# Kernel optimization log

Hardware: AMD Instinct MI355X
Metric: run time of the kernel (lower is better)

## Reference

```python
import jax, jax.numpy as jnp
import numpy as np

N_NODES = 50000


def gcn_conv(x, W, b, src, dst, n):
    # dense transform first (as PyG GCNConv does), then sparse aggregate
    h = x @ W  # [N, out]
    # add self loops
    loop = jnp.arange(n, dtype=src.dtype)
    s = jnp.concatenate([src, loop])
    d = jnp.concatenate([dst, loop])
    # symmetric normalization: deg over targets with unit edge weights
    deg = jax.ops.segment_sum(jnp.ones_like(d, dtype=h.dtype), d, num_segments=n)
    dinv = jnp.where(deg > 0, jax.lax.rsqrt(deg), 0.0)
    norm = dinv[s] * dinv[d]  # [E+N]
    msg = h[s] * norm[:, None]  # gather + scale
    out = jax.ops.segment_sum(msg, d, num_segments=n)  # scatter-add
    return out + b


def setup_inputs() -> dict:
    key = jax.random.key(0)
    k1, k2, k3, k4, k5 = jax.random.split(key, 5)
    in_dim, hid, out_dim = 256, 128, 16
    x = jax.random.normal(k1, (N_NODES, in_dim), dtype=jnp.float32)
    edge_index = jax.random.randint(k2, (2, 800000), 0, N_NODES, dtype=jnp.int64)
    # Glorot-style init for GCNConv weights, zero bias (PyG default)
    W1 = jax.random.normal(k3, (in_dim, hid), dtype=jnp.float32) / np.sqrt(in_dim)
    b1 = jnp.zeros((hid,), dtype=jnp.float32)
    W2 = jax.random.normal(k4, (hid, out_dim), dtype=jnp.float32) / np.sqrt(hid)
    b2 = jnp.zeros((out_dim,), dtype=jnp.float32)
    return {"x": x, "edge_index": edge_index, "W1": W1, "b1": b1, "W2": W2, "b2": b2}


def reference(x, edge_index, W1, b1, W2, b2):
    # eval-mode forward: dropout is identity
    src, dst = edge_index[0], edge_index[1]
    n = x.shape[0]
    h = gcn_conv(x, W1, b1, src, dst, n)
    h = jax.nn.relu(h)
    h = gcn_conv(h, W2, b2, src, dst, n)
    return jax.nn.log_softmax(h, axis=1)
```

## Files before the change

### kernel.cpp

```cpp
#include <hip/hip_runtime.h>
#include <hip/hip_bf16.h>

#define N_NODES 50000
#define E_EDGES 800000
#define IN_DIM  256
#define HID     128
#define OUT_DIM 16

#define NBUCK 391
#define NBLK  128
#define P2CAP 4096

using frag_ab = __attribute__((ext_vector_type(8))) short;
using frag_cd = __attribute__((ext_vector_type(4))) float;

static __device__ inline short f2bf(float f) {
    union { float f; unsigned u; } v; v.f = f;
    unsigned r = (v.u + 0x7fffu + ((v.u >> 16) & 1u)) >> 16;
    return (short)r;
}
static __device__ inline float bflo(unsigned u) {
    union { unsigned u; float f; } v; v.u = u << 16; return v.f;
}
static __device__ inline float bfhi(unsigned u) {
    union { unsigned u; float f; } v; v.u = u & 0xffff0000u; return v.f;
}
static __device__ inline unsigned packbf(float a, float b) {
    return (unsigned)(unsigned short)f2bf(a) | ((unsigned)(unsigned short)f2bf(b) << 16);
}


__global__ __launch_bounds__(256) void csr_a(const int4* __restrict__ dst4,
                                             int* __restrict__ cnt_bb) {
    __shared__ int h[NBUCK];
    int t = threadIdx.x;
    for (int i = t; i < NBUCK; i += 256) h[i] = 0;
    __syncthreads();
    for (int i = blockIdx.x * 256 + t; i < E_EDGES / 4; i += NBLK * 256) {
        int4 d = dst4[i];
        atomicAdd(&h[d.x >> 7], 1);
        atomicAdd(&h[d.y >> 7], 1);
        atomicAdd(&h[d.z >> 7], 1);
        atomicAdd(&h[d.w >> 7], 1);
    }
    __syncthreads();
    for (int i = t; i < NBUCK; i += 256) cnt_bb[i * NBLK + blockIdx.x] = h[i];
}

__global__ __launch_bounds__(NBLK) void csr_b1(int* __restrict__ cnt_bb,
                                               int* __restrict__ btot) {
    __shared__ int sm[NBLK];
    int b = blockIdx.x, t = threadIdx.x;
    int v = cnt_bb[b * NBLK + t];
    sm[t] = v;
    __syncthreads();
    for (int o = 1; o < NBLK; o <<= 1) {
        int u = (t >= o) ? sm[t - o] : 0;
        __syncthreads();
        sm[t] += u;
        __syncthreads();
    }
    cnt_bb[b * NBLK + t] = sm[t] - v;
    if (t == NBLK - 1) btot[b] = sm[t];
}

__global__ __launch_bounds__(512) void csr_b2(const int* __restrict__ btot,
                                              int* __restrict__ bbase) {
    __shared__ int sm[512];
    int t = threadIdx.x;
    int v = (t < NBUCK) ? btot[t] : 0;
    sm[t] = v;
    __syncthreads();
    for (int o = 1; o < 512; o <<= 1) {
        int u = (t >= o) ? sm[t - o] : 0;
        __syncthreads();
        sm[t] += u;
        __syncthreads();
    }
    if (t < NBUCK) bbase[t] = sm[t] - v;
    if (t == 511) bbase[NBUCK] = sm[511];
}

__global__ __launch_bounds__(256) void csr_c(const int4* __restrict__ src4,
                                             const int4* __restrict__ dst4,
                                             const int* __restrict__ cnt_bb,
                                             const int* __restrict__ bbase,
                                             unsigned* __restrict__ tmp) {
    __shared__ int run[NBUCK];
    int t = threadIdx.x;
    for (int i = t; i < NBUCK; i += 256)
        run[i] = bbase[i] + cnt_bb[i * NBLK + blockIdx.x];
    __syncthreads();
    for (int i = blockIdx.x * 256 + t; i < E_EDGES / 4; i += NBLK * 256) {
        int4 d = dst4[i];
        int4 s = src4[i];
        int p0 = atomicAdd(&run[d.x >> 7], 1);
        tmp[p0] = (unsigned)s.x | ((unsigned)(d.x & 127) << 17);
        int p1 = atomicAdd(&run[d.y >> 7], 1);
        tmp[p1] = (unsigned)s.y | ((unsigned)(d.y & 127) << 17);
        int p2 = atomicAdd(&run[d.z >> 7], 1);
        tmp[p2] = (unsigned)s.z | ((unsigned)(d.z & 127) << 17);
        int p3 = atomicAdd(&run[d.w >> 7], 1);
        tmp[p3] = (unsigned)s.w | ((unsigned)(d.w & 127) << 17);
    }
}

__global__ __launch_bounds__(256) void csr_p2(const unsigned* __restrict__ tmp,
                                              const int* __restrict__ bbase,
                                              int* __restrict__ rowptr,
                                              float* __restrict__ dinv,
                                              int* __restrict__ ssrc) {
    __shared__ unsigned ed[P2CAP];
    __shared__ int cnt[128];
    __shared__ int off[128];
    int b = blockIdx.x, t = threadIdx.x;
    int base = bbase[b];
    int m = bbase[b + 1] - base;
    if (m > P2CAP) m = P2CAP;
    if (t < 128) cnt[t] = 0;
    __syncthreads();
    for (int i = t; i < m; i += 256) {
        unsigned v = tmp[base + i];
        ed[i] = v;
        atomicAdd(&cnt[v >> 17], 1);
    }
    __syncthreads();
    if (t < 128) off[t] = cnt[t];
    __syncthreads();
    for (int o = 1; o < 128; o <<= 1) {
        int u = (t >= o && t < 128) ? off[t - o] : 0;
        __syncthreads();
        if (t < 128) off[t] += u;
        __syncthreads();
    }
    if (t < 128) {
        int node = b * 128 + t;
        int ex = off[t] - cnt[t];
        if (node < N_NODES) {
            rowptr[node] = base + ex;
            dinv[node] = rsqrtf((float)(cnt[t] + 1));
        }
        off[t] = ex;
    }
    if (b == NBUCK - 1 && t == 0) rowptr[N_NODES] = E_EDGES;
    __syncthreads();
    for (int i = t; i < m; i += 256) {
        unsigned v = ed[i];
        int p = atomicAdd(&off[v >> 17], 1);
        ssrc[base + p] = (int)(v & 0x1FFFF);
    }
}

__global__ void w1_transpose(const float* __restrict__ W, uint4* __restrict__ wtf) {
    int j = blockIdx.x * blockDim.x + threadIdx.x;
    if (j >= 64 * 64) return;
    int f = j >> 6, lane = j & 63;
    int kt = f >> 3, t = f & 7;
    int m = lane & 15, q = lane >> 4;
    int c = t * 16 + m;
    int k0 = kt * 32 + q * 8;
    unsigned p[4];
#pragma unroll
    for (int i = 0; i < 4; ++i)
        p[i] = packbf(W[(k0 + 2 * i) * HID + c], W[(k0 + 2 * i + 1) * HID + c]);
    uint4 v; v.x = p[0]; v.y = p[1]; v.z = p[2]; v.w = p[3];
    wtf[j] = v;
}

__global__ __launch_bounds__(512) void gemm1_mfma(const float* __restrict__ x,
                                                  const uint4* __restrict__ wtf,
                                                  const float* __restrict__ dinv,
                                                  short* __restrict__ h) {
    __shared__ uint4 lwt[64 * 64];
    int tid = threadIdx.x;
#pragma unroll
    for (int i = 0; i < 8; ++i)
        lwt[i * 512 + tid] = wtf[i * 512 + tid];

    int wave = tid >> 6;
    int lane = tid & 63;
    int m = lane & 15;
    int q = lane >> 4;
    int row0 = blockIdx.x * 128 + wave * 16;
    int arow_idx = row0 + m;
    const float4* arow4 = (const float4*)(x + (size_t)(arow_idx < N_NODES ? arow_idx : 0) * IN_DIM);

    frag_ab a[8];
#pragma unroll
    for (int kt = 0; kt < 8; ++kt) {
        float4 f0 = arow4[kt * 8 + q * 2];
        float4 f1 = arow4[kt * 8 + q * 2 + 1];
        a[kt][0] = f2bf(f0.x); a[kt][1] = f2bf(f0.y); a[kt][2] = f2bf(f0.z); a[kt][3] = f2bf(f0.w);
        a[kt][4] = f2bf(f1.x); a[kt][5] = f2bf(f1.y); a[kt][6] = f2bf(f1.z); a[kt][7] = f2bf(f1.w);
    }

    frag_cd acc[8];
#pragma unroll
    for (int t = 0; t < 8; ++t) acc[t] = frag_cd{0.f, 0.f, 0.f, 0.f};

    __syncthreads();

#pragma unroll
    for (int kt = 0; kt < 8; ++kt) {
#pragma unroll
        for (int t = 0; t < 8; ++t) {
            frag_ab b = *(const frag_ab*)&lwt[(kt * 8 + t) * 64 + lane];
            acc[t] = __builtin_amdgcn_mfma_f32_16x16x32_bf16(a[kt], b, acc[t], 0, 0, 0);
        }
    }

    float dv[4];
#pragma unroll
    for (int r = 0; r < 4; ++r) {
        int orow = row0 + q * 4 + r;
        dv[r] = (orow < N_NODES) ? dinv[orow] : 0.f;
    }
#pragma unroll
    for (int t = 0; t < 8; ++t) {
#pragma unroll
        for (int r = 0; r < 4; ++r) {
            int orow = row0 + q * 4 + r;
            if (orow < N_NODES)
                h[(size_t)orow * HID + t * 16 + m] = f2bf(acc[t][r] * dv[r]);
        }
    }
}

__global__ __launch_bounds__(256) void agg1_pull(const short* __restrict__ h1s,
                                                 const float* __restrict__ dinv,
                                                 const float* __restrict__ b1,
                                                 const int* __restrict__ rowptr,
                                                 const int* __restrict__ ssrc,
                                                 unsigned* __restrict__ out1) {
    int wave = threadIdx.x >> 6;
    int lane = threadIdx.x & 63;
    int node = __builtin_amdgcn_readfirstlane(blockIdx.x * 4 + wave);
    if (node >= N_NODES) return;
    int eo = lane >> 4;
    int g  = lane & 15;

    int lo = rowptr[node], hi = rowptr[node + 1];
    float a0 = 0.f, a1 = 0.f, a2 = 0.f, a3 = 0.f;
    float a4 = 0.f, a5 = 0.f, a6 = 0.f, a7 = 0.f;

    if (eo == 0) {
        uint4 u = *(const uint4*)(h1s + (size_t)node * HID + g * 8);
        a0 = bflo(u.x); a1 = bfhi(u.x); a2 = bflo(u.y); a3 = bfhi(u.y);
        a4 = bflo(u.z); a5 = bfhi(u.z); a6 = bflo(u.w); a7 = bfhi(u.w);
    }

    int e = lo;
#pragma unroll 2
    for (; e + 4 <= hi; e += 4) {
        int s = ssrc[e + eo];
        uint4 u = *(const uint4*)(h1s + (size_t)s * HID + g * 8);
        a0 += bflo(u.x); a1 += bfhi(u.x); a2 += bflo(u.y); a3 += bfhi(u.y);
        a4 += bflo(u.z); a5 += bfhi(u.z); a6 += bflo(u.w); a7 += bfhi(u.w);
    }
    if (eo < hi - e) {
        int s = ssrc[e + eo];
        uint4 u = *(const uint4*)(h1s + (size_t)s * HID + g * 8);
        a0 += bflo(u.x); a1 += bfhi(u.x); a2 += bflo(u.y); a3 += bfhi(u.y);
        a4 += bflo(u.z); a5 += bfhi(u.z); a6 += bflo(u.w); a7 += bfhi(u.w);
    }

    a0 += __shfl_xor(a0, 16); a1 += __shfl_xor(a1, 16);
    a2 += __shfl_xor(a2, 16); a3 += __shfl_xor(a3, 16);
    a4 += __shfl_xor(a4, 16); a5 += __shfl_xor(a5, 16);
    a6 += __shfl_xor(a6, 16); a7 += __shfl_xor(a7, 16);
    a0 += __shfl_xor(a0, 32); a1 += __shfl_xor(a1, 32);
    a2 += __shfl_xor(a2, 32); a3 += __shfl_xor(a3, 32);
    a4 += __shfl_xor(a4, 32); a5 += __shfl_xor(a5, 32);
    a6 += __shfl_xor(a6, 32); a7 += __shfl_xor(a7, 32);

    if (eo == 0) {
        float dd = dinv[node];
        float4 bA = *(const float4*)(b1 + g * 8);
        float4 bB = *(const float4*)(b1 + g * 8 + 4);
        float o0 = fmaxf(fmaf(dd, a0, bA.x), 0.f);
        float o1 = fmaxf(fmaf(dd, a1, bA.y), 0.f);
        float o2 = fmaxf(fmaf(dd, a2, bA.z), 0.f);
        float o3 = fmaxf(fmaf(dd, a3, bA.w), 0.f);
        float o4 = fmaxf(fmaf(dd, a4, bB.x), 0.f);
        float o5 = fmaxf(fmaf(dd, a5, bB.y), 0.f);
        float o6 = fmaxf(fmaf(dd, a6, bB.z), 0.f);
        float o7 = fmaxf(fmaf(dd, a7, bB.w), 0.f);
        uint4 st;
        st.x = packbf(o0, o1); st.y = packbf(o2, o3);
        st.z = packbf(o4, o5); st.w = packbf(o6, o7);
        *(uint4*)(out1 + (size_t)node * (HID / 2) + g * 4) = st;
    }
}

__global__ void gemm2_kernel(const unsigned* __restrict__ h, const float* __restrict__ W,
                             const float* __restrict__ dinv, float* __restrict__ out, int n) {
    int idx = blockIdx.x * blockDim.x + threadIdx.x;
    if (idx >= n * 4) return;
    int node = idx >> 2;
    int f4 = (idx & 3) << 2;
    const uint2* hr = (const uint2*)(h + (size_t)node * (HID / 2));
    float4 acc = {0.f, 0.f, 0.f, 0.f};
#pragma unroll 8
    for (int k = 0; k < HID; k += 4) {
        uint2 u = hr[k >> 2];
        float x0 = bflo(u.x), x1 = bfhi(u.x), x2 = bflo(u.y), x3 = bfhi(u.y);
        float4 w0 = *(const float4*)(W + (k + 0) * OUT_DIM + f4);
        float4 w1 = *(const float4*)(W + (k + 1) * OUT_DIM + f4);
        float4 w2 = *(const float4*)(W + (k + 2) * OUT_DIM + f4);
        float4 w3 = *(const float4*)(W + (k + 3) * OUT_DIM + f4);
        acc.x += x0 * w0.x + x1 * w1.x + x2 * w2.x + x3 * w3.x;
        acc.y += x0 * w0.y + x1 * w1.y + x2 * w2.y + x3 * w3.y;
        acc.z += x0 * w0.z + x1 * w1.z + x2 * w2.z + x3 * w3.z;
        acc.w += x0 * w0.w + x1 * w1.w + x2 * w2.w + x3 * w3.w;
    }
    float dv = dinv[node];
    acc.x *= dv; acc.y *= dv; acc.z *= dv; acc.w *= dv;
    *(float4*)(out + (size_t)node * OUT_DIM + f4) = acc;
}

__global__ __launch_bounds__(256) void agg2_pull(const float* __restrict__ h2s,
                                                 const float* __restrict__ dinv,
                                                 const float* __restrict__ b2,
                                                 const int* __restrict__ rowptr,
                                                 const int* __restrict__ ssrc,
                                                 float* __restrict__ out) {
    int wave = threadIdx.x >> 6;
    int lane = threadIdx.x & 63;
    int node = __builtin_amdgcn_readfirstlane(blockIdx.x * 4 + wave);
    if (node >= N_NODES) return;
    int eo = lane >> 4;
    int f  = lane & 15;

    int lo = rowptr[node], hi = rowptr[node + 1];
    float acc = (eo == 0) ? h2s[(size_t)node * OUT_DIM + f] : 0.f;

    int e = lo;
#pragma unroll 2
    for (; e + 4 <= hi; e += 4)
        acc += h2s[(size_t)ssrc[e + eo] * OUT_DIM + f];
    if (e + eo < hi)
        acc += h2s[(size_t)ssrc[e + eo] * OUT_DIM + f];

    acc += __shfl_xor(acc, 16);
    acc += __shfl_xor(acc, 32);

    float dd = dinv[node];
    float v = fmaf(dd, acc, b2[f]);

    float m = v;
#pragma unroll
    for (int msk = 1; msk < 16; msk <<= 1) m = fmaxf(m, __shfl_xor(m, msk));
    float ex = __expf(v - m);
    float ssum = ex;
#pragma unroll
    for (int msk = 1; msk < 16; msk <<= 1) ssum += __shfl_xor(ssum, msk);
    if (eo == 0) out[(size_t)node * OUT_DIM + f] = v - m - __logf(ssum);
}

extern "C" void kernel_launch(void* const* d_in, const int* in_sizes, int n_in,
                              void* d_out, int out_size, void* d_ws, size_t ws_size,
                              hipStream_t stream) {
    const float* x  = (const float*)d_in[0];
    const int*   ei = (const int*)d_in[1];
    const float* W1 = (const float*)d_in[2];
    const float* b1 = (const float*)d_in[3];
    const float* W2 = (const float*)d_in[4];
    const float* b2 = (const float*)d_in[5];
    float* out = (float*)d_out;

    const int n = N_NODES;
    const int e = E_EDGES;
    const int* srcp = ei;
    const int* dstp = ei + e;

    char* w = (char*)d_ws;
    int*      cnt_bb = (int*)w;        w += (size_t)NBUCK * NBLK * 4;
    int*      btot   = (int*)w;        w += (size_t)NBUCK * 4;
    int*      bbase  = (int*)w;        w += (size_t)(NBUCK + 1) * 4;
    int*      rowptr = (int*)w;        w += (size_t)(n + 1) * 4;
    float*    dinv   = (float*)w;      w += (size_t)n * 4;
    unsigned* tmp    = (unsigned*)w;   w += (size_t)e * 4;
    int*      ssrc   = (int*)w;        w += (size_t)e * 4;
    uint4*    wtf    = (uint4*)w;      w += (size_t)64 * 64 * 16;
    short*    h1s    = (short*)w;      w += (size_t)n * HID * 2;
    unsigned* out1   = (unsigned*)w;   w += (size_t)n * HID * 2;
    float*    h2s    = (float*)w;      w += (size_t)n * OUT_DIM * 4;

    const int B = 256;
    auto blk = [](long long total, int b) { return (int)((total + b - 1) / b); };

    csr_a<<<NBLK, 256, 0, stream>>>((const int4*)dstp, cnt_bb);
    csr_b1<<<NBUCK, NBLK, 0, stream>>>(cnt_bb, btot);
    csr_b2<<<1, 512, 0, stream>>>(btot, bbase);
    csr_c<<<NBLK, 256, 0, stream>>>((const int4*)srcp, (const int4*)dstp, cnt_bb, bbase, tmp);
    csr_p2<<<NBUCK, 256, 0, stream>>>(tmp, bbase, rowptr, dinv, ssrc);

    w1_transpose<<<16, 256, 0, stream>>>(W1, wtf);
    gemm1_mfma<<<blk(n, 128), 512, 0, stream>>>(x, wtf, dinv, h1s);
    agg1_pull<<<blk(n, 4), 256, 0, stream>>>(h1s, dinv, b1, rowptr, ssrc, out1);

    gemm2_kernel<<<blk((long long)n * 4, B), B, 0, stream>>>(out1, W2, dinv, h2s, n);
    agg2_pull<<<blk(n, 4), 256, 0, stream>>>(h2s, dinv, b2, rowptr, ssrc, out);
}
```

Measured before the change: 207.4 us.

## Fuse layer-2 dense transform into layer-1 aggregation and merge W1 transpose launch

```diff
diff --git a/kernel.cpp b/kernel.cpp
--- a/kernel.cpp
+++ b/kernel.cpp
@@ -64,10 +64,27 @@
     if (t == NBLK - 1) btot[b] = sm[t];
 }
 
-__global__ __launch_bounds__(512) void csr_b2(const int* __restrict__ btot,
-                                              int* __restrict__ bbase) {
+__global__ __launch_bounds__(512) void csr_b2_w1t(const int* __restrict__ btot,
+                                                  int* __restrict__ bbase,
+                                                  const float* __restrict__ W,
+                                                  uint4* __restrict__ wtf) {
+    int t = threadIdx.x;
+    if (blockIdx.x < 8) {
+        int j = blockIdx.x * 512 + t;
+        int f = j >> 6, lane = j & 63;
+        int kt = f >> 3, tt = f & 7;
+        int m = lane & 15, q = lane >> 4;
+        int c = tt * 16 + m;
+        int k0 = kt * 32 + q * 8;
+        unsigned p[4];
+#pragma unroll
+        for (int i = 0; i < 4; ++i)
+            p[i] = packbf(W[(k0 + 2 * i) * HID + c], W[(k0 + 2 * i + 1) * HID + c]);
+        uint4 v; v.x = p[0]; v.y = p[1]; v.z = p[2]; v.w = p[3];
+        wtf[j] = v;
+        return;
+    }
     __shared__ int sm[512];
-    int t = threadIdx.x;
     int v = (t < NBUCK) ? btot[t] : 0;
     sm[t] = v;
     __syncthreads();
@@ -151,22 +168,6 @@
     }
 }
 
-__global__ void w1_transpose(const float* __restrict__ W, uint4* __restrict__ wtf) {
-    int j = blockIdx.x * blockDim.x + threadIdx.x;
-    if (j >= 64 * 64) return;
-    int f = j >> 6, lane = j & 63;
-    int kt = f >> 3, t = f & 7;
-    int m = lane & 15, q = lane >> 4;
-    int c = t * 16 + m;
-    int k0 = kt * 32 + q * 8;
-    unsigned p[4];
-#pragma unroll
-    for (int i = 0; i < 4; ++i)
-        p[i] = packbf(W[(k0 + 2 * i) * HID + c], W[(k0 + 2 * i + 1) * HID + c]);
-    uint4 v; v.x = p[0]; v.y = p[1]; v.z = p[2]; v.w = p[3];
-    wtf[j] = v;
-}
-
 __global__ __launch_bounds__(512) void gemm1_mfma(const float* __restrict__ x,
                                                   const uint4* __restrict__ wtf,
                                                   const float* __restrict__ dinv,
@@ -226,14 +227,22 @@
     }
 }
 
-__global__ __launch_bounds__(256) void agg1_pull(const short* __restrict__ h1s,
-                                                 const float* __restrict__ dinv,
-                                                 const float* __restrict__ b1,
-                                                 const int* __restrict__ rowptr,
-                                                 const int* __restrict__ ssrc,
-                                                 unsigned* __restrict__ out1) {
-    int wave = threadIdx.x >> 6;
-    int lane = threadIdx.x & 63;
+__global__ __launch_bounds__(256) void agg1_fused(const short* __restrict__ h1s,
+                                                  const float* __restrict__ dinv,
+                                                  const float* __restrict__ b1,
+                                                  const float* __restrict__ W2,
+                                                  const int* __restrict__ rowptr,
+                                                  const int* __restrict__ ssrc,
+                                                  float* __restrict__ h2s) {
+    __shared__ float sw2[HID * OUT_DIM];
+    __shared__ float srow[4][HID];
+    int tid = threadIdx.x;
+#pragma unroll
+    for (int i = 0; i < 8; ++i) sw2[i * 256 + tid] = W2[i * 256 + tid];
+    __syncthreads();
+
+    int wave = tid >> 6;
+    int lane = tid & 63;
     int node = __builtin_amdgcn_readfirstlane(blockIdx.x * 4 + wave);
     if (node >= N_NODES) return;
     int eo = lane >> 4;
@@ -273,49 +282,30 @@
     a4 += __shfl_xor(a4, 32); a5 += __shfl_xor(a5, 32);
     a6 += __shfl_xor(a6, 32); a7 += __shfl_xor(a7, 32);
 
+    float dd = dinv[node];
     if (eo == 0) {
-        float dd = dinv[node];
         float4 bA = *(const float4*)(b1 + g * 8);
         float4 bB = *(const float4*)(b1 + g * 8 + 4);
-        float o0 = fmaxf(fmaf(dd, a0, bA.x), 0.f);
-        float o1 = fmaxf(fmaf(dd, a1, bA.y), 0.f);
-        float o2 = fmaxf(fmaf(dd, a2, bA.z), 0.f);
-        float o3 = fmaxf(fmaf(dd, a3, bA.w), 0.f);
-        float o4 = fmaxf(fmaf(dd, a4, bB.x), 0.f);
-        float o5 = fmaxf(fmaf(dd, a5, bB.y), 0.f);
-        float o6 = fmaxf(fmaf(dd, a6, bB.z), 0.f);
-        float o7 = fmaxf(fmaf(dd, a7, bB.w), 0.f);
-        uint4 st;
-        st.x = packbf(o0, o1); st.y = packbf(o2, o3);
-        st.z = packbf(o4, o5); st.w = packbf(o6, o7);
-        *(uint4*)(out1 + (size_t)node * (HID / 2) + g * 4) = st;
-    }
-}
-
-__global__ void gemm2_kernel(const unsigned* __restrict__ h, const float* __restrict__ W,
-                             const float* __restrict__ dinv, float* __restrict__ out, int n) {
-    int idx = blockIdx.x * blockDim.x + threadIdx.x;
-    if (idx >= n * 4) return;
-    int node = idx >> 2;
-    int f4 = (idx & 3) << 2;
-    const uint2* hr = (const uint2*)(h + (size_t)node * (HID / 2));
-    float4 acc = {0.f, 0.f, 0.f, 0.f};
+        float* sr = srow[wave] + g * 8;
+        sr[0] = fmaxf(fmaf(dd, a0, bA.x), 0.f);
+        sr[1] = fmaxf(fmaf(dd, a1, bA.y), 0.f);
+        sr[2] = fmaxf(fmaf(dd, a2, bA.z), 0.f);
+        sr[3] = fmaxf(fmaf(dd, a3, bA.w), 0.f);
+        sr[4] = fmaxf(fmaf(dd, a4, bB.x), 0.f);
+        sr[5] = fmaxf(fmaf(dd, a5, bB.y), 0.f);
+        sr[6] = fmaxf(fmaf(dd, a6, bB.z), 0.f);
+        sr[7] = fmaxf(fmaf(dd, a7, bB.w), 0.f);
+    }
+    const float* sr = srow[wave];
+    float p = 0.f;
 #pragma unroll 8
-    for (int k = 0; k < HID; k += 4) {
-        uint2 u = hr[k >> 2];
-        float x0 = bflo(u.x), x1 = bfhi(u.x), x2 = bflo(u.y), x3 = bfhi(u.y);
-        float4 w0 = *(const float4*)(W + (k + 0) * OUT_DIM + f4);
-        float4 w1 = *(const float4*)(W + (k + 1) * OUT_DIM + f4);
-        float4 w2 = *(const float4*)(W + (k + 2) * OUT_DIM + f4);
-        float4 w3 = *(const float4*)(W + (k + 3) * OUT_DIM + f4);
-        acc.x += x0 * w0.x + x1 * w1.x + x2 * w2.x + x3 * w3.x;
-        acc.y += x0 * w0.y + x1 * w1.y + x2 * w2.y + x3 * w3.y;
-        acc.z += x0 * w0.z + x1 * w1.z + x2 * w2.z + x3 * w3.z;
-        acc.w += x0 * w0.w + x1 * w1.w + x2 * w2.w + x3 * w3.w;
-    }
-    float dv = dinv[node];
-    acc.x *= dv; acc.y *= dv; acc.z *= dv; acc.w *= dv;
-    *(float4*)(out + (size_t)node * OUT_DIM + f4) = acc;
+    for (int kk = 0; kk < 32; ++kk) {
+        int k = eo * 32 + kk;
+        p = fmaf(sr[k], sw2[k * OUT_DIM + g], p);
+    }
+    p += __shfl_xor(p, 16);
+    p += __shfl_xor(p, 32);
+    if (eo == 0) h2s[(size_t)node * OUT_DIM + g] = p * dd;
 }
 
 __global__ __launch_bounds__(256) void agg2_pull(const float* __restrict__ h2s,
@@ -383,22 +373,18 @@
     int*      ssrc   = (int*)w;        w += (size_t)e * 4;
     uint4*    wtf    = (uint4*)w;      w += (size_t)64 * 64 * 16;
     short*    h1s    = (short*)w;      w += (size_t)n * HID * 2;
-    unsigned* out1   = (unsigned*)w;   w += (size_t)n * HID * 2;
     float*    h2s    = (float*)w;      w += (size_t)n * OUT_DIM * 4;
 
-    const int B = 256;
     auto blk = [](long long total, int b) { return (int)((total + b - 1) / b); };
 
     csr_a<<<NBLK, 256, 0, stream>>>((const int4*)dstp, cnt_bb);
     csr_b1<<<NBUCK, NBLK, 0, stream>>>(cnt_bb, btot);
-    csr_b2<<<1, 512, 0, stream>>>(btot, bbase);
+    csr_b2_w1t<<<9, 512, 0, stream>>>(btot, bbase, W1, wtf);
     csr_c<<<NBLK, 256, 0, stream>>>((const int4*)srcp, (const int4*)dstp, cnt_bb, bbase, tmp);
     csr_p2<<<NBUCK, 256, 0, stream>>>(tmp, bbase, rowptr, dinv, ssrc);
 
-    w1_transpose<<<16, 256, 0, stream>>>(W1, wtf);
     gemm1_mfma<<<blk(n, 128), 512, 0, stream>>>(x, wtf, dinv, h1s);
-    agg1_pull<<<blk(n, 4), 256, 0, stream>>>(h1s, dinv, b1, rowptr, ssrc, out1);
-
-    gemm2_kernel<<<blk((long long)n * 4, B), B, 0, stream>>>(out1, W2, dinv, h2s, n);
+    agg1_fused<<<blk(n, 4), 256, 0, stream>>>(h1s, dinv, b1, W2, rowptr, ssrc, h2s);
+
     agg2_pull<<<blk(n, 4), 256, 0, stream>>>(h2s, dinv, b2, rowptr, ssrc, out);
 }
```

Result: faster. 199.4 us (-3.8%).
